# Kernel tuning notes

Measured on AMD Instinct MI355X. Metric: run time of the kernel, lower is better.

The kernel has to match this reference:

```python
import jax, jax.numpy as jnp
import numpy as np

FEAT_DIM = 256
NUM_HEADS = 4
GATE_HID = FEAT_DIM // 4
LN_EPS = 1e-5


def setup_inputs() -> dict:
    key = jax.random.key(0)
    ks = jax.random.split(key, 12)
    C, H = FEAT_DIM, NUM_HEADS
    s = 1.0 / np.sqrt(C)
    inp = {
        "features": jax.random.normal(ks[0], (8, 16384, C), dtype=jnp.float32),
        "view_proj_w": jax.random.normal(ks[1], (C, C), dtype=jnp.float32) * s,
        "view_proj_b": jnp.zeros((C,), dtype=jnp.float32),
        "in_proj_w": jax.random.normal(ks[2], (3 * C, C), dtype=jnp.float32) * s,
        "in_proj_b": jnp.zeros((3 * C,), dtype=jnp.float32),
        "out_proj_w": jax.random.normal(ks[3], (C, C), dtype=jnp.float32) * s,
        "out_proj_b": jnp.zeros((C,), dtype=jnp.float32),
        "gate_w1": jax.random.normal(ks[4], (GATE_HID, C), dtype=jnp.float32) * s,
        "gate_b1": jnp.zeros((GATE_HID,), dtype=jnp.float32),
        "gate_w2": jax.random.normal(ks[5], (1, GATE_HID), dtype=jnp.float32) * (1.0 / np.sqrt(GATE_HID)),
        "gate_b2": jnp.zeros((1,), dtype=jnp.float32),
        "ln_g": jnp.ones((C,), dtype=jnp.float32),
        "ln_b": jnp.zeros((C,), dtype=jnp.float32),
    }
    return inp


def reference(features, view_proj_w, view_proj_b, in_proj_w, in_proj_b,
              out_proj_w, out_proj_b, gate_w1, gate_b1, gate_w2, gate_b2,
              ln_g, ln_b):
    N, L, C = features.shape
    H = NUM_HEADS
    D = C // H

    # view embedding: scalar id/N broadcast over C, then Linear  -> [N,1,C]
    view_ids = (jnp.arange(N, dtype=features.dtype) / N)[:, None, None]  # [N,1,1]
    view_vec = jnp.broadcast_to(view_ids, (N, 1, C))
    view_info = view_vec @ view_proj_w.T + view_proj_b                    # [N,1,C]
    view_features = features + view_info                                  # [N,L,C]

    tokens = jnp.transpose(view_features, (1, 0, 2))                      # [L,N,C]

    # batched tiny cross-view self-attention: batch=L, seq=N
    qkv = tokens @ in_proj_w.T + in_proj_b                                # [L,N,3C]
    q, k, v = jnp.split(qkv, 3, axis=-1)
    q = q.reshape(L, N, H, D)
    k = k.reshape(L, N, H, D)
    v = v.reshape(L, N, H, D)
    scores = jnp.einsum("lnhd,lmhd->lhnm", q, k) / jnp.sqrt(jnp.array(D, features.dtype))
    attn = jax.nn.softmax(scores, axis=-1)                                # [L,H,N,N]
    ctx = jnp.einsum("lhnm,lmhd->lnhd", attn, v).reshape(L, N, C)
    attended = ctx @ out_proj_w.T + out_proj_b                            # [L,N,C]

    # gated softmax aggregation over views
    g = jax.nn.relu(attended @ gate_w1.T + gate_b1)                       # [L,N,C/4]
    g = jax.nn.sigmoid(g @ gate_w2.T + gate_b2)[..., 0]                   # [L,N]
    w = jax.nn.softmax(g, axis=-1)                                        # [L,N]
    fused = jnp.einsum("lnc,ln->lc", attended, w)[None]                   # [1,L,C]

    # LayerNorm over C
    mu = fused.mean(-1, keepdims=True)
    var = fused.var(-1, keepdims=True)
    fused = (fused - mu) * jax.lax.rsqrt(var + LN_EPS) * ln_g + ln_b
    return fused
```

## Files before the change

### kernel.cpp

```cpp
#include <hip/hip_runtime.h>

#define L_DIM 16384
#define C_DIM 256
#define NV 8
#define NH 4
#define DH 64
#define TL 4
#define NTHREADS 256

#define QKP 132
#define VVP 68
#define GPAD 65

typedef __attribute__((ext_vector_type(8))) _Float16 f16x8;
typedef __attribute__((ext_vector_type(4))) float f32x4;

__global__ void prep_kernel(const float* __restrict__ vw, const float* __restrict__ vb,
                            const float* __restrict__ w_in, const float* __restrict__ w_out,
                            const float* __restrict__ w_g1,
                            float* __restrict__ view_info, _Float16* __restrict__ win_pk,
                            _Float16* __restrict__ wout_pk, _Float16* __restrict__ wg1_pk){
  int tid = threadIdx.x, bid = blockIdx.x;
  if (bid == 0){
    int c = tid;
    const float4* vr = (const float4*)(vw + c*C_DIM);
    float rs = 0.f;
#pragma unroll 8
    for (int k = 0; k < 64; k++){ float4 x = vr[k]; rs += x.x + x.y + x.z + x.w; }
    float b = vb[c];
    for (int n = 0; n < NV; n++) view_info[n*C_DIM + c] = (n * 0.125f) * rs + b;
  }
  int gid = bid * blockDim.x + tid;
  int stride = gridDim.x * blockDim.x;
  const int NWIN = 24576, NWOUT = 8192, NWG = 2048;
  for (int f = gid; f < NWIN + NWOUT + NWG; f += stride){
    if (f < NWIN){
      int lane = f & 63, kc = (f>>6)&7, nt = (f>>9)&3, pc = f>>11;
      int p = pc % 3, h = pc / 3;
      int row = p*C_DIM + h*DH + nt*16 + (lane&15);
      int col = (lane>>4)*8 + kc*32;
      const float* src = w_in + (long)row*C_DIM + col;
      _Float16* d = win_pk + (long)f*8;
#pragma unroll
      for (int j = 0; j < 8; j++) d[j] = (_Float16)src[j];
    } else if (f < NWIN + NWOUT){
      int f2 = f - NWIN;
      int lane = f2 & 63, kc = (f2>>6)&7, nt = (f2>>9)&3, cc = f2>>11;
      int row = cc*64 + nt*16 + (lane&15);
      int col = (lane>>4)*8 + kc*32;
      const float* src = w_out + (long)row*C_DIM + col;
      _Float16* d = wout_pk + (long)f2*8;
#pragma unroll
      for (int j = 0; j < 8; j++) d[j] = (_Float16)src[j];
    } else {
      int f3 = f - NWIN - NWOUT;
      int lane = f3 & 63, kc = (f3>>6)&7, nt = (f3>>9)&3;
      int row = nt*16 + (lane&15);
      int col = (lane>>4)*8 + kc*32;
      const float* src = w_g1 + (long)row*C_DIM + col;
      _Float16* d = wg1_pk + (long)f3*8;
#pragma unroll
      for (int j = 0; j < 8; j++) d[j] = (_Float16)src[j];
    }
  }
}

__global__ __launch_bounds__(NTHREADS, 3)
void fused_kernel(const float* __restrict__ feat,
                  const float* __restrict__ view_info,
                  const _Float16* __restrict__ win,
                  const _Float16* __restrict__ wout,
                  const _Float16* __restrict__ wg1,
                  const float* __restrict__ b_in,
                  const float* __restrict__ b_out,
                  const float* __restrict__ b_g1,
                  const float* __restrict__ w2,
                  const float* __restrict__ b2,
                  const float* __restrict__ ln_g,
                  const float* __restrict__ ln_b,
                  float* __restrict__ out)
{
  extern __shared__ char smem[];
  _Float16* A   = (_Float16*)smem;
  _Float16* att = (_Float16*)smem;
  _Float16* qk  = (_Float16*)(smem + 16384);
  float*    g1s = (float*)(smem + 16384);
  _Float16* vv  = (_Float16*)(smem + 24832);
  _Float16* ctx = (_Float16*)(smem + 29184);
  float* gl   = (float*)(smem + 45568);
  float* wgt  = gl + 32;
  float* red1 = wgt + 32;
  float* red2 = red1 + 128;
  float* mus  = red2 + 128;
  float* rvs  = mus + 4;

  const int tid  = threadIdx.x;
  const int wv   = tid >> 6, lane = tid & 63;
  const int quad = lane >> 4, l15 = lane & 15;

  {
    int row = tid >> 3, j = tid & 7;
    int n = row & 7, lloc = row >> 3;
    long l = (long)blockIdx.x * TL + lloc;
    const float* fb = feat + ((long)n * L_DIM + l) * C_DIM + j*32;
    const float* vb = view_info + n * C_DIM + j*32;
    _Float16* arow = A + row*256;
#pragma unroll
    for (int i = 0; i < 4; i++){
      float4 x0 = *(const float4*)(fb + i*8);
      float4 x1 = *(const float4*)(fb + i*8 + 4);
      float4 v0 = *(const float4*)(vb + i*8);
      float4 v1 = *(const float4*)(vb + i*8 + 4);
      f16x8 hf;
      hf[0] = (_Float16)(x0.x+v0.x); hf[1] = (_Float16)(x0.y+v0.y);
      hf[2] = (_Float16)(x0.z+v0.z); hf[3] = (_Float16)(x0.w+v0.w);
      hf[4] = (_Float16)(x1.x+v1.x); hf[5] = (_Float16)(x1.y+v1.y);
      hf[6] = (_Float16)(x1.z+v1.z); hf[7] = (_Float16)(x1.w+v1.w);
      int s = j*4 + i;
      *(f16x8*)(arow + ((s ^ row))*8) = hf;
    }
  }
  __syncthreads();

  for (int h = 0; h < NH; h++){
    if (h) __syncthreads();
    {
      const _Float16* bp = win + (long)(h*96 + wv*8)*512 + lane*8;
      f32x4 z = {0.f,0.f,0.f,0.f};
      f32x4 acc[3][2];
#pragma unroll
      for (int p = 0; p < 3; p++){ acc[p][0] = z; acc[p][1] = z; }
#pragma unroll
      for (int kc = 0; kc < 8; kc++){
        int s0 = quad + 4*kc;
        int r1 = 16 + l15;
        f16x8 a0 = *(const f16x8*)(A + l15*256 + ((s0 ^ l15))*8);
        f16x8 a1 = *(const f16x8*)(A + r1*256  + ((s0 ^ r1))*8);
#pragma unroll
        for (int p = 0; p < 3; p++){
          f16x8 b = *(const f16x8*)(bp + (p*32 + kc)*512);
          acc[p][0] = __builtin_amdgcn_mfma_f32_16x16x32_f16(a0, b, acc[p][0], 0,0,0);
          acc[p][1] = __builtin_amdgcn_mfma_f32_16x16x32_f16(a1, b, acc[p][1], 0,0,0);
        }
      }
      int colc = wv*16 + l15;
#pragma unroll
      for (int p = 0; p < 2; p++){
        float bias = b_in[p*C_DIM + h*DH + colc];
#pragma unroll
        for (int r = 0; r < 4; r++){
          qk[(quad*4 + r)*QKP + p*64 + colc]      = (_Float16)(acc[p][0][r] + bias);
          qk[(16 + quad*4 + r)*QKP + p*64 + colc] = (_Float16)(acc[p][1][r] + bias);
        }
      }
      {
        float bias = b_in[2*C_DIM + h*DH + colc];
#pragma unroll
        for (int r = 0; r < 4; r++){
          vv[(quad*4 + r)*VVP + colc]      = (_Float16)(acc[2][0][r] + bias);
          vv[(16 + quad*4 + r)*VVP + colc] = (_Float16)(acc[2][1][r] + bias);
        }
      }
    }
    __syncthreads();
    {
      int nn = lane >> 3, mm = lane & 7;
      int tq = wv*8 + nn;
      const _Float16* qrow = qk + tq*QKP;
      const _Float16* krow = qk + (wv*8 + mm)*QKP + 64;
      float s = 0.f;
#pragma unroll
      for (int d8 = 0; d8 < 8; d8++){
        f16x8 q8 = *(const f16x8*)(qrow + d8*8);
        f16x8 k8 = *(const f16x8*)(krow + d8*8);
#pragma unroll
        for (int j = 0; j < 8; j++) s += (float)q8[j] * (float)k8[j];
      }
      s *= 0.125f;
      float mx = s;
#pragma unroll
      for (int o = 1; o < 8; o <<= 1) mx = fmaxf(mx, __shfl_xor(mx, o));
      float e = __expf(s - mx);
      float sum = e;
#pragma unroll
      for (int o = 1; o < 8; o <<= 1) sum += __shfl_xor(sum, o);
      float attnw = e / sum;
      float c8[8] = {0,0,0,0,0,0,0,0};
#pragma unroll
      for (int mp = 0; mp < 8; mp++){
        float aw = __shfl(attnw, (nn<<3) | mp);
        f16x8 v8 = *(const f16x8*)(vv + (wv*8 + mp)*VVP + mm*8);
#pragma unroll
        for (int j = 0; j < 8; j++) c8[j] += aw * (float)v8[j];
      }
      f16x8 cp;
#pragma unroll
      for (int j = 0; j < 8; j++) cp[j] = (_Float16)c8[j];
      int slot = h*8 + mm;
      *(f16x8*)(ctx + tq*256 + ((slot ^ (tq & 31)))*8) = cp;
    }
  }
  __syncthreads();

  {
    f32x4 z = {0.f,0.f,0.f,0.f};
    f32x4 acc[4][2];
#pragma unroll
    for (int nt = 0; nt < 4; nt++){ acc[nt][0] = z; acc[nt][1] = z; }
#pragma unroll
    for (int kc = 0; kc < 8; kc++){
      int s0 = quad + 4*kc;
      int r1 = 16 + l15;
      f16x8 a0 = *(const f16x8*)(ctx + l15*256 + ((s0 ^ l15))*8);
      f16x8 a1 = *(const f16x8*)(ctx + r1*256  + ((s0 ^ r1))*8);
#pragma unroll
      for (int nt = 0; nt < 4; nt++){
        f16x8 b = *(const f16x8*)(wout + (long)((wv*32 + nt*8 + kc)*512) + lane*8);
        acc[nt][0] = __builtin_amdgcn_mfma_f32_16x16x32_f16(a0, b, acc[nt][0], 0,0,0);
        acc[nt][1] = __builtin_amdgcn_mfma_f32_16x16x32_f16(a1, b, acc[nt][1], 0,0,0);
      }
    }
#pragma unroll
    for (int nt = 0; nt < 4; nt++){
      int col = wv*64 + nt*16 + l15;
      float bias = b_out[col];
      int slot = col >> 3, j = col & 7;
#pragma unroll
      for (int r = 0; r < 4; r++){
        int row0 = quad*4 + r, row1 = 16 + quad*4 + r;
        att[row0*256 + ((slot ^ row0))*8 + j] = (_Float16)(acc[nt][0][r] + bias);
        att[row1*256 + ((slot ^ row1))*8 + j] = (_Float16)(acc[nt][1][r] + bias);
      }
    }
  }
  __syncthreads();

  {
    f32x4 acc0 = {0.f,0.f,0.f,0.f}, acc1 = {0.f,0.f,0.f,0.f};
#pragma unroll
    for (int kc = 0; kc < 8; kc++){
      int s0 = quad + 4*kc;
      int r1 = 16 + l15;
      f16x8 a0 = *(const f16x8*)(att + l15*256 + ((s0 ^ l15))*8);
      f16x8 a1 = *(const f16x8*)(att + r1*256  + ((s0 ^ r1))*8);
      f16x8 b = *(const f16x8*)(wg1 + (long)((wv*8 + kc)*512) + lane*8);
      acc0 = __builtin_amdgcn_mfma_f32_16x16x32_f16(a0, b, acc0, 0,0,0);
      acc1 = __builtin_amdgcn_mfma_f32_16x16x32_f16(a1, b, acc1, 0,0,0);
    }
    int col = wv*16 + l15;
    float bias = b_g1[col];
#pragma unroll
    for (int r = 0; r < 4; r++){
      g1s[(quad*4 + r)*GPAD + col]      = fmaxf(acc0[r] + bias, 0.f);
      g1s[(16 + quad*4 + r)*GPAD + col] = fmaxf(acc1[r] + bias, 0.f);
    }
  }
  __syncthreads();

  {
    int t = tid >> 3, part = tid & 7;
    const float* g1r = g1s + t*GPAD + part*8;
    const float* w2p = w2 + part*8;
    float s = 0.f;
#pragma unroll
    for (int j = 0; j < 8; j++) s += g1r[j] * w2p[j];
    s += __shfl_xor(s, 1);
    s += __shfl_xor(s, 2);
    s += __shfl_xor(s, 4);
    if (part == 0) gl[t] = 1.f / (1.f + __expf(-(s + b2[0])));
  }
  __syncthreads();
  if (tid < 4){
    float v[8]; float mx = -1e30f;
    for (int n = 0; n < 8; n++){ v[n] = gl[tid*8+n]; mx = fmaxf(mx, v[n]); }
    float sum = 0.f;
    for (int n = 0; n < 8; n++){ v[n] = __expf(v[n]-mx); sum += v[n]; }
    float inv = 1.f/sum;
    for (int n = 0; n < 8; n++) wgt[tid*8+n] = v[n]*inv;
  }
  __syncthreads();

  float f8[8];
  const int lfl = tid >> 5, ccf = tid & 31;
  if (tid < 128){
    float wloc[8];
#pragma unroll
    for (int n = 0; n < 8; n++) wloc[n] = wgt[lfl*8+n];
#pragma unroll
    for (int j = 0; j < 8; j++) f8[j] = 0.f;
#pragma unroll
    for (int n = 0; n < 8; n++){
      int row = lfl*8 + n;
      f16x8 a8 = *(const f16x8*)(att + row*256 + ((ccf ^ row))*8);
      float aw = wloc[n];
#pragma unroll
      for (int j = 0; j < 8; j++) f8[j] += aw * (float)a8[j];
    }
    float s = 0.f, s2 = 0.f;
#pragma unroll
    for (int j = 0; j < 8; j++){ s += f8[j]; s2 += f8[j]*f8[j]; }
    red1[lfl*32 + ccf] = s;
    red2[lfl*32 + ccf] = s2;
  }
  __syncthreads();
  if (tid < 4){
    float s = 0.f, s2 = 0.f;
    for (int i = 0; i < 32; i++){ s += red1[tid*32+i]; s2 += red2[tid*32+i]; }
    float mu = s * (1.f/256.f);
    float var = s2 * (1.f/256.f) - mu*mu;
    mus[tid] = mu;
    rvs[tid] = rsqrtf(var + 1e-5f);
  }
  __syncthreads();
  if (tid < 128){
    float mu = mus[lfl], rv = rvs[lfl];
    long lg = (long)blockIdx.x * TL + lfl;
    float* op = out + lg * C_DIM + ccf*8;
    float o8[8];
#pragma unroll
    for (int j = 0; j < 8; j++){
      int c = ccf*8 + j;
      o8[j] = (f8[j]-mu)*rv*ln_g[c] + ln_b[c];
    }
    *(float4*)(op)   = make_float4(o8[0],o8[1],o8[2],o8[3]);
    *(float4*)(op+4) = make_float4(o8[4],o8[5],o8[6],o8[7]);
  }
}

extern "C" void kernel_launch(void* const* d_in, const int* in_sizes, int n_in,
                              void* d_out, int out_size, void* d_ws, size_t ws_size,
                              hipStream_t stream){
  const float* feat  = (const float*)d_in[0];
  const float* vw    = (const float*)d_in[1];
  const float* vb    = (const float*)d_in[2];
  const float* w_in  = (const float*)d_in[3];
  const float* b_in  = (const float*)d_in[4];
  const float* w_out = (const float*)d_in[5];
  const float* b_out = (const float*)d_in[6];
  const float* w_g1  = (const float*)d_in[7];
  const float* b_g1  = (const float*)d_in[8];
  const float* w2    = (const float*)d_in[9];
  const float* b2    = (const float*)d_in[10];
  const float* lng   = (const float*)d_in[11];
  const float* lnb   = (const float*)d_in[12];

  char* ws = (char*)d_ws;
  float*    view_info = (float*)ws;
  _Float16* win_pk  = (_Float16*)(ws + 8192);
  _Float16* wout_pk = (_Float16*)(ws + 401408);
  _Float16* wg1_pk  = (_Float16*)(ws + 532480);

  prep_kernel<<<256, 256, 0, stream>>>(vw, vb, w_in, w_out, w_g1,
                                       view_info, win_pk, wout_pk, wg1_pk);
  fused_kernel<<<L_DIM/TL, NTHREADS, 46880, stream>>>(
      feat, view_info, win_pk, wout_pk, wg1_pk,
      b_in, b_out, b_g1, w2, b2, lng, lnb, (float*)d_out);
}
```

Before: 487.8 us.

## Prefetch weights into registers, shrink LDS, transpose MFMA outputs, use fdot2

Several changes to the fused cross-view attention kernel. It double-buffers weight fragments for the QKV, out-proj and gate GEMMs in registers so global loads overlap the MFMAs. It keeps per-head context vectors in registers until the last head, which lets the LDS regions overlap and cuts shared memory from about 46KB to 32KB, and it raises launch bounds to 4 blocks. It swaps the MFMA operand order so each lane writes packed f16x4/float4 results, and uses fdot2 for the Q·K dot products. The extra live registers may cause spills under the tighter launch bound.

```diff
diff --git a/kernel.cpp b/kernel.cpp
--- a/kernel.cpp
+++ b/kernel.cpp
@@ -10,10 +10,14 @@
 
 #define QKP 132
 #define VVP 68
-#define GPAD 65
+#define GPAD 68
 
 typedef __attribute__((ext_vector_type(8))) _Float16 f16x8;
+typedef __attribute__((ext_vector_type(4))) _Float16 f16x4;
+typedef __attribute__((ext_vector_type(2))) _Float16 f16x2;
 typedef __attribute__((ext_vector_type(4))) float f32x4;
+
+union F8u { f16x8 v; f16x2 p[4]; };
 
 __global__ void prep_kernel(const float* __restrict__ vw, const float* __restrict__ vb,
                             const float* __restrict__ w_in, const float* __restrict__ w_out,
@@ -65,7 +69,7 @@
   }
 }
 
-__global__ __launch_bounds__(NTHREADS, 3)
+__global__ __launch_bounds__(NTHREADS, 4)
 void fused_kernel(const float* __restrict__ feat,
                   const float* __restrict__ view_info,
                   const _Float16* __restrict__ win,
@@ -82,21 +86,39 @@
 {
   extern __shared__ char smem[];
   _Float16* A   = (_Float16*)smem;
-  _Float16* att = (_Float16*)smem;
-  _Float16* qk  = (_Float16*)(smem + 16384);
-  float*    g1s = (float*)(smem + 16384);
-  _Float16* vv  = (_Float16*)(smem + 24832);
-  _Float16* ctx = (_Float16*)(smem + 29184);
-  float* gl   = (float*)(smem + 45568);
+  _Float16* ctx = (_Float16*)smem;
+  float*    g1s = (float*)smem;
+  float* gl   = (float*)(smem + 8704);
   float* wgt  = gl + 32;
   float* red1 = wgt + 32;
   float* red2 = red1 + 128;
   float* mus  = red2 + 128;
   float* rvs  = mus + 4;
+  _Float16* qk  = (_Float16*)(smem + 16384);
+  _Float16* vv  = (_Float16*)(smem + 24832);
+  _Float16* att = (_Float16*)(smem + 16384);
 
   const int tid  = threadIdx.x;
   const int wv   = tid >> 6, lane = tid & 63;
   const int quad = lane >> 4, l15 = lane & 15;
+
+  const _Float16* wbin  = win  + (long)(wv*8)*512 + lane*8;
+  const _Float16* wbout = wout + (long)(wv*32)*512 + lane*8;
+  const _Float16* wbg1  = wg1  + (long)(wv*8)*512 + lane*8;
+
+#define QSET(dst, g) do { int h_=(g)>>3, kc_=(g)&7; \
+  dst[0] = *(const f16x8*)(wbin + ((h_*3+0)*32 + kc_)*512); \
+  dst[1] = *(const f16x8*)(wbin + ((h_*3+1)*32 + kc_)*512); \
+  dst[2] = *(const f16x8*)(wbin + ((h_*3+2)*32 + kc_)*512); } while(0)
+#define OSET(dst, kc) do { \
+  dst[0] = *(const f16x8*)(wbout + (0*8+(kc))*512); \
+  dst[1] = *(const f16x8*)(wbout + (1*8+(kc))*512); \
+  dst[2] = *(const f16x8*)(wbout + (2*8+(kc))*512); \
+  dst[3] = *(const f16x8*)(wbout + (3*8+(kc))*512); } while(0)
+
+  f16x8 wz[2][3];
+  QSET(wz[0], 0);
+  QSET(wz[1], 1);
 
   {
     int row = tid >> 3, j = tid & 7;
@@ -122,48 +144,55 @@
   }
   __syncthreads();
 
+  f16x8 wo[2][4];
+  f16x8 wg[8];
+  f16x8 cpk0, cpk1, cpk2;
+
+#pragma unroll
   for (int h = 0; h < NH; h++){
     if (h) __syncthreads();
     {
-      const _Float16* bp = win + (long)(h*96 + wv*8)*512 + lane*8;
       f32x4 z = {0.f,0.f,0.f,0.f};
       f32x4 acc[3][2];
 #pragma unroll
       for (int p = 0; p < 3; p++){ acc[p][0] = z; acc[p][1] = z; }
 #pragma unroll
       for (int kc = 0; kc < 8; kc++){
+        int g = h*8 + kc;
         int s0 = quad + 4*kc;
         int r1 = 16 + l15;
         f16x8 a0 = *(const f16x8*)(A + l15*256 + ((s0 ^ l15))*8);
         f16x8 a1 = *(const f16x8*)(A + r1*256  + ((s0 ^ r1))*8);
 #pragma unroll
         for (int p = 0; p < 3; p++){
-          f16x8 b = *(const f16x8*)(bp + (p*32 + kc)*512);
-          acc[p][0] = __builtin_amdgcn_mfma_f32_16x16x32_f16(a0, b, acc[p][0], 0,0,0);
-          acc[p][1] = __builtin_amdgcn_mfma_f32_16x16x32_f16(a1, b, acc[p][1], 0,0,0);
+          acc[p][0] = __builtin_amdgcn_mfma_f32_16x16x32_f16(wz[g&1][p], a0, acc[p][0], 0,0,0);
+          acc[p][1] = __builtin_amdgcn_mfma_f32_16x16x32_f16(wz[g&1][p], a1, acc[p][1], 0,0,0);
         }
-      }
-      int colc = wv*16 + l15;
-#pragma unroll
-      for (int p = 0; p < 2; p++){
-        float bias = b_in[p*C_DIM + h*DH + colc];
+        if (g + 2 <= 31) QSET(wz[g&1], g+2);
+      }
+      int c4 = wv*16 + quad*4;
+#pragma unroll
+      for (int p = 0; p < 3; p++){
+        float4 b4 = *(const float4*)(b_in + p*C_DIM + h*DH + c4);
+        float bb[4] = {b4.x, b4.y, b4.z, b4.w};
+        f16x4 s0, s1;
 #pragma unroll
         for (int r = 0; r < 4; r++){
-          qk[(quad*4 + r)*QKP + p*64 + colc]      = (_Float16)(acc[p][0][r] + bias);
-          qk[(16 + quad*4 + r)*QKP + p*64 + colc] = (_Float16)(acc[p][1][r] + bias);
+          s0[r] = (_Float16)(acc[p][0][r] + bb[r]);
+          s1[r] = (_Float16)(acc[p][1][r] + bb[r]);
         }
-      }
-      {
-        float bias = b_in[2*C_DIM + h*DH + colc];
-#pragma unroll
-        for (int r = 0; r < 4; r++){
-          vv[(quad*4 + r)*VVP + colc]      = (_Float16)(acc[2][0][r] + bias);
-          vv[(16 + quad*4 + r)*VVP + colc] = (_Float16)(acc[2][1][r] + bias);
+        if (p < 2){
+          *(f16x4*)(qk + l15*QKP      + p*64 + c4) = s0;
+          *(f16x4*)(qk + (16+l15)*QKP + p*64 + c4) = s1;
+        } else {
+          *(f16x4*)(vv + l15*VVP      + c4) = s0;
+          *(f16x4*)(vv + (16+l15)*VVP + c4) = s1;
         }
       }
     }
     __syncthreads();
     {
+      if (h == 3){ OSET(wo[0], 0); OSET(wo[1], 1); }
       int nn = lane >> 3, mm = lane & 7;
       int tq = wv*8 + nn;
       const _Float16* qrow = qk + tq*QKP;
@@ -171,10 +200,17 @@
       float s = 0.f;
 #pragma unroll
       for (int d8 = 0; d8 < 8; d8++){
-        f16x8 q8 = *(const f16x8*)(qrow + d8*8);
-        f16x8 k8 = *(const f16x8*)(krow + d8*8);
-#pragma unroll
-        for (int j = 0; j < 8; j++) s += (float)q8[j] * (float)k8[j];
+        F8u q8, k8;
+        q8.v = *(const f16x8*)(qrow + d8*8);
+        k8.v = *(const f16x8*)(krow + d8*8);
+#if __has_builtin(__builtin_amdgcn_fdot2)
+#pragma unroll
+        for (int j2 = 0; j2 < 4; j2++)
+          s = __builtin_amdgcn_fdot2(q8.p[j2], k8.p[j2], s, false);
+#else
+#pragma unroll
+        for (int j = 0; j < 8; j++) s += (float)q8.v[j] * (float)k8.v[j];
+#endif
       }
       s *= 0.125f;
       float mx = s;
@@ -196,8 +232,16 @@
       f16x8 cp;
 #pragma unroll
       for (int j = 0; j < 8; j++) cp[j] = (_Float16)c8[j];
-      int slot = h*8 + mm;
-      *(f16x8*)(ctx + tq*256 + ((slot ^ (tq & 31)))*8) = cp;
+      if (h == 0)      cpk0 = cp;
+      else if (h == 1) cpk1 = cp;
+      else if (h == 2) cpk2 = cp;
+      else {
+        _Float16* crow = ctx + tq*256;
+        *(f16x8*)(crow + ((( 0 + mm) ^ tq))*8) = cpk0;
+        *(f16x8*)(crow + ((( 8 + mm) ^ tq))*8) = cpk1;
+        *(f16x8*)(crow + (((16 + mm) ^ tq))*8) = cpk2;
+        *(f16x8*)(crow + (((24 + mm) ^ tq))*8) = cp;
+      }
     }
   }
   __syncthreads();
@@ -215,23 +259,28 @@
       f16x8 a1 = *(const f16x8*)(ctx + r1*256  + ((s0 ^ r1))*8);
 #pragma unroll
       for (int nt = 0; nt < 4; nt++){
-        f16x8 b = *(const f16x8*)(wout + (long)((wv*32 + nt*8 + kc)*512) + lane*8);
-        acc[nt][0] = __builtin_amdgcn_mfma_f32_16x16x32_f16(a0, b, acc[nt][0], 0,0,0);
-        acc[nt][1] = __builtin_amdgcn_mfma_f32_16x16x32_f16(a1, b, acc[nt][1], 0,0,0);
-      }
+        acc[nt][0] = __builtin_amdgcn_mfma_f32_16x16x32_f16(wo[kc&1][nt], a0, acc[nt][0], 0,0,0);
+        acc[nt][1] = __builtin_amdgcn_mfma_f32_16x16x32_f16(wo[kc&1][nt], a1, acc[nt][1], 0,0,0);
+      }
+      if (kc < 6) OSET(wo[kc&1], kc+2);
     }
 #pragma unroll
     for (int nt = 0; nt < 4; nt++){
-      int col = wv*64 + nt*16 + l15;
-      float bias = b_out[col];
-      int slot = col >> 3, j = col & 7;
+      int c4 = wv*64 + nt*16 + quad*4;
+      float4 b4 = *(const float4*)(b_out + c4);
+      float bb[4] = {b4.x, b4.y, b4.z, b4.w};
+      f16x4 s0, s1;
 #pragma unroll
       for (int r = 0; r < 4; r++){
-        int row0 = quad*4 + r, row1 = 16 + quad*4 + r;
-        att[row0*256 + ((slot ^ row0))*8 + j] = (_Float16)(acc[nt][0][r] + bias);
-        att[row1*256 + ((slot ^ row1))*8 + j] = (_Float16)(acc[nt][1][r] + bias);
-      }
-    }
+        s0[r] = (_Float16)(acc[nt][0][r] + bb[r]);
+        s1[r] = (_Float16)(acc[nt][1][r] + bb[r]);
+      }
+      int slot = c4 >> 3, jo = c4 & 7;
+      *(f16x4*)(att + l15*256      + ((slot ^ l15))*8      + jo) = s0;
+      *(f16x4*)(att + (16+l15)*256 + ((slot ^ (16+l15)))*8 + jo) = s1;
+    }
+#pragma unroll
+    for (int kc = 0; kc < 8; kc++) wg[kc] = *(const f16x8*)(wbg1 + kc*512);
   }
   __syncthreads();
 
@@ -243,17 +292,19 @@
       int r1 = 16 + l15;
       f16x8 a0 = *(const f16x8*)(att + l15*256 + ((s0 ^ l15))*8);
       f16x8 a1 = *(const f16x8*)(att + r1*256  + ((s0 ^ r1))*8);
-      f16x8 b = *(const f16x8*)(wg1 + (long)((wv*8 + kc)*512) + lane*8);
-      acc0 = __builtin_amdgcn_mfma_f32_16x16x32_f16(a0, b, acc0, 0,0,0);
-      acc1 = __builtin_amdgcn_mfma_f32_16x16x32_f16(a1, b, acc1, 0,0,0);
-    }
-    int col = wv*16 + l15;
-    float bias = b_g1[col];
-#pragma unroll
-    for (int r = 0; r < 4; r++){
-      g1s[(quad*4 + r)*GPAD + col]      = fmaxf(acc0[r] + bias, 0.f);
-      g1s[(16 + quad*4 + r)*GPAD + col] = fmaxf(acc1[r] + bias, 0.f);
-    }
+      acc0 = __builtin_amdgcn_mfma_f32_16x16x32_f16(wg[kc], a0, acc0, 0,0,0);
+      acc1 = __builtin_amdgcn_mfma_f32_16x16x32_f16(wg[kc], a1, acc1, 0,0,0);
+    }
+    int c4 = wv*16 + quad*4;
+    float4 b4 = *(const float4*)(b_g1 + c4);
+    float bb[4] = {b4.x, b4.y, b4.z, b4.w};
+    float4 o0, o1;
+    o0.x = fmaxf(acc0[0]+bb[0], 0.f); o0.y = fmaxf(acc0[1]+bb[1], 0.f);
+    o0.z = fmaxf(acc0[2]+bb[2], 0.f); o0.w = fmaxf(acc0[3]+bb[3], 0.f);
+    o1.x = fmaxf(acc1[0]+bb[0], 0.f); o1.y = fmaxf(acc1[1]+bb[1], 0.f);
+    o1.z = fmaxf(acc1[2]+bb[2], 0.f); o1.w = fmaxf(acc1[3]+bb[3], 0.f);
+    *(float4*)(g1s + l15*GPAD      + c4) = o0;
+    *(float4*)(g1s + (16+l15)*GPAD + c4) = o1;
   }
   __syncthreads();
 
@@ -352,7 +403,7 @@
 
   prep_kernel<<<256, 256, 0, stream>>>(vw, vb, w_in, w_out, w_g1,
                                        view_info, win_pk, wout_pk, wg1_pk);
-  fused_kernel<<<L_DIM/TL, NTHREADS, 46880, stream>>>(
+  fused_kernel<<<L_DIM/TL, NTHREADS, 32768, stream>>>(
       feat, view_info, win_pk, wout_pk, wg1_pk,
       b_in, b_out, b_g1, w2, b2, lng, lnb, (float*)d_out);
 }
```

After: 434.9 us. 1.12x faster.
